# Performance work log

Measured on AMD Instinct MI355X. Metric: run time of the kernel, lower is better.

Reference implementation:

```python
import jax, jax.numpy as jnp
import numpy as np

N_HEAD = 9
HEAD_DIM = 64
KV_PER_HEAD = 21  # 189 // 9
ROPE_BASE = 10000.0


def _rotate_half(x):
    # matches torch: x1 = first half (floor), x2 = rest; cat(-x2, x1)
    h = x.shape[-1] // 2
    return jnp.concatenate([-x[..., h:], x[..., :h]], axis=-1)


def _rope_cos_sin(T, dtype):
    inv_freq = 1.0 / (ROPE_BASE ** (jnp.arange(0, KV_PER_HEAD, 2, dtype=jnp.float32) / KV_PER_HEAD))  # [11]
    t = jnp.arange(T, dtype=jnp.float32)
    freqs = jnp.einsum('i,j->ij', t, inv_freq)          # [T, 11]
    emb = jnp.concatenate([freqs, freqs], axis=-1)      # [T, 22]
    cos = jnp.cos(emb)[:, :KV_PER_HEAD].astype(dtype)   # [T, 21]
    sin = jnp.sin(emb)[:, :KV_PER_HEAD].astype(dtype)
    return cos, sin


def setup_inputs() -> dict:
    key = jax.random.key(0)
    ks = jax.random.split(key, 5)
    B, T, C = 4, 2048, 576
    kv_dim = 189
    s = 0.02
    return {
        'x': jax.random.normal(ks[0], (B, T, C), dtype=jnp.float32),
        'Wq': jax.random.normal(ks[1], (C, C), dtype=jnp.float32) * s,
        'Wk': jax.random.normal(ks[2], (C, kv_dim), dtype=jnp.float32) * s,
        'Wv': jax.random.normal(ks[3], (C, kv_dim), dtype=jnp.float32) * s,
        'Wo': jax.random.normal(ks[4], (C, C), dtype=jnp.float32) * s,
    }


def reference(x, Wq, Wk, Wv, Wo):
    B, T, C = x.shape
    q = (x @ Wq).reshape(B, T, N_HEAD, HEAD_DIM).transpose(0, 2, 1, 3)      # [B,H,T,64]
    k = (x @ Wk).reshape(B, T, N_HEAD, KV_PER_HEAD).transpose(0, 2, 1, 3)   # [B,H,T,21]
    v = (x @ Wv).reshape(B, T, N_HEAD, KV_PER_HEAD).transpose(0, 2, 1, 3)   # [B,H,T,21]

    cos, sin = _rope_cos_sin(T, x.dtype)  # [T,21] each, broadcasts over B,H
    k_rot = k * cos + _rotate_half(k) * sin
    q_part = q[..., :KV_PER_HEAD]
    q_rot_part = q_part * cos + _rotate_half(q_part) * sin
    # q dims >= KV_PER_HEAD never touch nonzero K, so only the first 21 dims matter
    scale = 1.0 / np.sqrt(HEAD_DIM)
    scores = jnp.einsum('bhqd,bhkd->bhqk', q_rot_part, k_rot) * scale       # [B,H,T,T]
    causal = jnp.tril(jnp.ones((T, T), dtype=bool))
    scores = jnp.where(causal, scores, -1e9)
    attn = jax.nn.softmax(scores, axis=-1)
    y_small = jnp.einsum('bhqk,bhkd->bhqd', attn, v)                        # [B,H,T,21]
    # zero-pad up to head_dim (matches k_pad/v_pad construction)
    y = jnp.pad(y_small, ((0, 0), (0, 0), (0, 0), (0, HEAD_DIM - KV_PER_HEAD)))
    y = y.transpose(0, 2, 1, 3).reshape(B, T, C)
    return y @ Wo
```

## Files before the change

### kernel.cpp

```cpp
#include <hip/hip_runtime.h>
#include <hip/hip_bf16.h>

typedef unsigned short u16;
typedef unsigned int u32;
typedef __attribute__((ext_vector_type(8))) short bf16x8;
typedef __attribute__((ext_vector_type(4))) float f32x4;
typedef __attribute__((ext_vector_type(4))) int i32x4;

#define N_HEADS 9
#define T_SEQ 2048
#define BATCH 4
#define CDIM 576
#define ROWS (BATCH * T_SEQ)
#define NBH (BATCH * N_HEADS)
#define PART_SLOT ((size_t)NBH * T_SEQ * 32)

__device__ __forceinline__ u16 f2bf(float f) {
    u32 u = __float_as_uint(f);
    u32 r = u + 0x7FFFu + ((u >> 16) & 1u);
    return (u16)(r >> 16);
}
__device__ __forceinline__ float bf2f(u16 u) { return __uint_as_float(((u32)u) << 16); }
__device__ __forceinline__ u32 cvt_pk_bf16(float lo, float hi) {
    u32 r;
    asm("v_cvt_pk_bf16_f32 %0, %1, %2" : "=v"(r) : "v"(lo), "v"(hi));
    return r;
}
__device__ __forceinline__ float exp2_raw(float x) {
    float r;
    asm("v_exp_f32 %0, %1" : "=v"(r) : "v"(x));
    return r;
}

__global__ __launch_bounds__(256) void prep_wt(const float* __restrict__ Wq, const float* __restrict__ Wk,
                                               const float* __restrict__ Wv, const float* __restrict__ Wo,
                                               u16* __restrict__ WcT, u16* __restrict__ WoSubT,
                                               float* __restrict__ cosT, float* __restrict__ sinT) {
    int idx = blockIdx.x * 256 + threadIdx.x;
    if (idx < 576 * 576) {
        int n = idx / 576, k = idx - n * 576;
        float v;
        if (n < 189)      v = Wq[(size_t)k * 576 + (n / 21) * 64 + (n % 21)];
        else if (n < 378) v = Wk[(size_t)k * 189 + (n - 189)];
        else if (n < 567) v = Wv[(size_t)k * 189 + (n - 378)];
        else              v = 0.f;
        WcT[(size_t)n * 576 + k] = f2bf(v);
    }
    if (idx < 576 * 192) {
        int n = idx / 192, k = idx - n * 192;
        float v = 0.f;
        if (k < 189) v = Wo[(size_t)((k / 21) * 64 + (k % 21)) * 576 + n];
        WoSubT[(size_t)n * 192 + k] = f2bf(v);
    }
    if (idx < T_SEQ * 21) {
        int t = idx / 21, d = idx - t * 21;
        int i = (d < 11) ? d : d - 11;
        float e = (2.0f * (float)i) / 21.0f;
        float invf = exp2f(-e * 13.287712379549449f);
        float ang = (float)t * invf;
        cosT[idx] = cosf(ang);
        sinT[idx] = sinf(ang);
    }
}


template <int AF32, int OUTF32>
__global__ __launch_bounds__(256) void gemm_mfma(const void* __restrict__ Av, const u16* __restrict__ BT,
                                                 void* __restrict__ Cout, int K, int lda, int ldbt, int ldc) {
    __shared__ u16 As[128][32];
    __shared__ u16 Bs[64][32];
    const int tid = threadIdx.x;
    const int lane = tid & 63, w = tid >> 6;
    const int m0 = blockIdx.x * 128, n0 = blockIdx.y * 64;
    const int k15 = lane & 15, g = lane >> 4;

    const int arow = tid >> 1;
    const int ac0 = (tid & 1) * 2;
    const int brow = tid >> 2, bc = tid & 3;

    f32x4 zero = {0.f, 0.f, 0.f, 0.f};
    f32x4 acc[2][4];
#pragma unroll
    for (int hf = 0; hf < 2; hf++)
#pragma unroll
        for (int n = 0; n < 4; n++) acc[hf][n] = zero;

    const float* Af = (const float*)Av;
    const u16*   Ab = (const u16*)Av;

    float4 af0, af1, af2, af3;
    i32x4 av0, av1;
    if (AF32) {
        const float* ap = &Af[(size_t)(m0 + arow) * lda + ac0 * 8];
        af0 = *(const float4*)&ap[0];
        af1 = *(const float4*)&ap[4];
        af2 = *(const float4*)&ap[8];
        af3 = *(const float4*)&ap[12];
    } else {
        av0 = *(const i32x4*)&Ab[(size_t)(m0 + arow) * lda + ac0 * 8];
        av1 = *(const i32x4*)&Ab[(size_t)(m0 + arow) * lda + (ac0 + 1) * 8];
    }
    i32x4 bv = *(const i32x4*)&BT[(size_t)(n0 + brow) * ldbt + bc * 8];

    for (int k0 = 0; k0 < K; k0 += 32) {
        __syncthreads();
        if (AF32) {
            i32x4 w0, w1;
            w0[0] = (int)cvt_pk_bf16(af0.x, af0.y); w0[1] = (int)cvt_pk_bf16(af0.z, af0.w);
            w0[2] = (int)cvt_pk_bf16(af1.x, af1.y); w0[3] = (int)cvt_pk_bf16(af1.z, af1.w);
            w1[0] = (int)cvt_pk_bf16(af2.x, af2.y); w1[1] = (int)cvt_pk_bf16(af2.z, af2.w);
            w1[2] = (int)cvt_pk_bf16(af3.x, af3.y); w1[3] = (int)cvt_pk_bf16(af3.z, af3.w);
            *(i32x4*)&As[arow][(ac0 ^ (arow & 3)) * 8] = w0;
            *(i32x4*)&As[arow][((ac0 + 1) ^ (arow & 3)) * 8] = w1;
        } else {
            *(i32x4*)&As[arow][(ac0 ^ (arow & 3)) * 8] = av0;
            *(i32x4*)&As[arow][((ac0 + 1) ^ (arow & 3)) * 8] = av1;
        }
        *(i32x4*)&Bs[brow][(bc ^ (brow & 3)) * 8] = bv;
        __syncthreads();
        int k1 = k0 + 32;
        if (k1 < K) {
            if (AF32) {
                const float* ap = &Af[(size_t)(m0 + arow) * lda + k1 + ac0 * 8];
                af0 = *(const float4*)&ap[0];
                af1 = *(const float4*)&ap[4];
                af2 = *(const float4*)&ap[8];
                af3 = *(const float4*)&ap[12];
            } else {
                av0 = *(const i32x4*)&Ab[(size_t)(m0 + arow) * lda + k1 + ac0 * 8];
                av1 = *(const i32x4*)&Ab[(size_t)(m0 + arow) * lda + k1 + (ac0 + 1) * 8];
            }
            bv = *(const i32x4*)&BT[(size_t)(n0 + brow) * ldbt + k1 + bc * 8];
        }
        const int ar0 = w * 32 + k15;
        bf16x8 a0 = *(const bf16x8*)&As[ar0][(g ^ (ar0 & 3)) * 8];
        bf16x8 a1 = *(const bf16x8*)&As[ar0 + 16][(g ^ (ar0 & 3)) * 8];
#pragma unroll
        for (int n = 0; n < 4; n++) {
            int br = n * 16 + k15;
            bf16x8 b = *(const bf16x8*)&Bs[br][(g ^ (br & 3)) * 8];
            acc[0][n] = __builtin_amdgcn_mfma_f32_16x16x32_bf16(a0, b, acc[0][n], 0, 0, 0);
            acc[1][n] = __builtin_amdgcn_mfma_f32_16x16x32_bf16(a1, b, acc[1][n], 0, 0, 0);
        }
    }
#pragma unroll
    for (int hf = 0; hf < 2; hf++)
#pragma unroll
        for (int n = 0; n < 4; n++)
#pragma unroll
            for (int i = 0; i < 4; i++) {
                int row = m0 + w * 32 + hf * 16 + g * 4 + i;
                int col = n0 + n * 16 + k15;
                float v = acc[hf][n][i];
                if (OUTF32) ((float*)Cout)[(size_t)row * ldc + col] = v;
                else        ((u16*)Cout)[(size_t)row * ldc + col] = f2bf(v);
            }
}


__global__ __launch_bounds__(256) void repack_qk(const u16* __restrict__ qkv,
                                                 const float* __restrict__ cosT,
                                                 const float* __restrict__ sinT,
                                                 u16* __restrict__ Qp, u16* __restrict__ Kp) {
    int gid = blockIdx.x * 256 + threadIdx.x;
    int c = gid & 3;
    int t = (gid >> 2) & 2047;
    int bh = gid >> 13;
    int b = bh / N_HEADS, h = bh - b * N_HEADS;
    const u16* qrow = qkv + (size_t)(b * T_SEQ + t) * CDIM + h * 21;
    const u16* krow = qrow + 189;
    const float* cr = cosT + t * 21;
    const float* sr = sinT + t * 21;
    u32 wq[4] = {0, 0, 0, 0}, wk[4] = {0, 0, 0, 0};
    const float sc = 0.18033688011112042f;
#pragma unroll
    for (int j = 0; j < 8; j++) {
        int d = c * 8 + j;
        float vq = 0.f, vk = 0.f;
        if (d < 21) {
            int pd = (d < 11) ? d + 10 : d - 11;
            float cc = cr[d], ss = sr[d];
            float qv = bf2f(qrow[d]), qp = bf2f(qrow[pd]);
            float kv = bf2f(krow[d]), kp = bf2f(krow[pd]);
            float rq = (d < 11) ? -qp : qp;
            float rk = (d < 11) ? -kp : kp;
            vq = (qv * cc + rq * ss) * sc;
            vk = kv * cc + rk * ss;
        }
        wq[j >> 1] |= (u32)f2bf(vq) << ((j & 1) * 16);
        wk[j >> 1] |= (u32)f2bf(vk) << ((j & 1) * 16);
    }
    size_t obase = ((size_t)bh * T_SEQ + t) * 32 + c * 8;
    i32x4 q4; q4[0] = (int)wq[0]; q4[1] = (int)wq[1]; q4[2] = (int)wq[2]; q4[3] = (int)wq[3];
    i32x4 k4; k4[0] = (int)wk[0]; k4[1] = (int)wk[1]; k4[2] = (int)wk[2]; k4[3] = (int)wk[3];
    *(i32x4*)&Qp[obase] = q4;
    *(i32x4*)&Kp[obase] = k4;
}

__global__ __launch_bounds__(256) void repack_v(const u16* __restrict__ qkv, u16* __restrict__ Vp) {
    __shared__ u16 Vs[256][26];
    const int tid = threadIdx.x;
    const int bh = blockIdx.y;
    const int b = bh / N_HEADS, h = bh - b * N_HEADS;
    const int t0 = blockIdx.x * 256;

    const u16* src = qkv + (size_t)(b * T_SEQ + t0 + tid) * CDIM + 378 + h * 21;
#pragma unroll
    for (int d = 0; d < 21; d++) Vs[tid][d] = src[d];
    __syncthreads();

    const int d = tid >> 3, tc = tid & 7;
    u32 wv[16];
#pragma unroll
    for (int j = 0; j < 32; j += 2) {
        u16 lo, hi;
        if (d < 21)      { lo = Vs[tc * 32 + j][d]; hi = Vs[tc * 32 + j + 1][d]; }
        else if (d == 31){ lo = 0x3F80; hi = 0x3F80; }
        else             { lo = 0; hi = 0; }
        wv[j >> 1] = (u32)lo | ((u32)hi << 16);
    }
    u16* dst = &Vp[((size_t)bh * 32 + d) * T_SEQ + t0 + tc * 32];
#pragma unroll
    for (int q = 0; q < 4; q++) {
        i32x4 v4; v4[0] = (int)wv[q*4]; v4[1] = (int)wv[q*4+1]; v4[2] = (int)wv[q*4+2]; v4[3] = (int)wv[q*4+3];
        *(i32x4*)&dst[q * 8] = v4;
    }
}


__global__ __launch_bounds__(256) void attn_mfma(const u16* __restrict__ Qp,
                                                 const u16* __restrict__ Kp,
                                                 const u16* __restrict__ Vp,
                                                 u16* __restrict__ Ybuf,
                                                 u16* __restrict__ Part) {
    __shared__ u16 Ks[128][40];
    __shared__ u16 Vt[32][136];
    __shared__ u16 Pt[4][16][72];
    const int tid = threadIdx.x;
    const int lane = tid & 63, w = tid >> 6;
    const int bh = blockIdx.y;
    const int b = bh / N_HEADS, h = bh - b * N_HEADS;
    const int k15 = lane & 15, g = lane >> 4;

    int bx = blockIdx.x, qt, ci;
    if (bx < 32) { qt = 31 - (bx >> 1); ci = bx & 1; }
    else         { qt = 47 - bx;        ci = 0;      }
    const int q0 = qt * 64;
    const int n64 = qt + 1;
    const int n128 = (n64 + 1) >> 1;
    int u_begin, u_end;
    if (qt < 16) { u_begin = 0; u_end = n128; }
    else { int c0 = (n128 + 1) >> 1; u_begin = ci ? c0 : 0; u_end = ci ? n128 : c0; }

    const u16* Kg = Kp + (((size_t)bh << 11) * 32) + (tid >> 1) * 32 + (tid & 1) * 16;
    const u16* Vg = Vp + (size_t)bh * 32 * T_SEQ + (size_t)(tid >> 3) * T_SEQ + (tid & 7) * 16;
    const int krow = tid >> 1, kcc = (tid & 1) * 16;
    const int vrow = tid >> 3, vcc = (tid & 7) * 16;

    bf16x8 qf = *(const bf16x8*)&Qp[(((size_t)bh << 11) + q0 + w * 16 + k15) * 32 + g * 8];

    f32x4 y0 = {0.f, 0.f, 0.f, 0.f}, y1 = {0.f, 0.f, 0.f, 0.f};
    const int qloc = w * 16 + k15;

    u32 ko = (u32)u_begin * 4096u;
    u32 vo = (u32)u_begin * 128u;
    i32x4 ka0 = *(const i32x4*)&Kg[ko];
    i32x4 ka1 = *(const i32x4*)&Kg[ko + 8];
    i32x4 va0 = *(const i32x4*)&Vg[vo];
    i32x4 va1 = *(const i32x4*)&Vg[vo + 8];

    for (int u = u_begin; u < u_end; ++u) {
        __syncthreads();
        *(i32x4*)&Ks[krow][kcc] = ka0;
        *(i32x4*)&Ks[krow][kcc + 8] = ka1;
        *(i32x4*)&Vt[vrow][vcc] = va0;
        *(i32x4*)&Vt[vrow][vcc + 8] = va1;
        if (u + 1 < u_end) {
            ko += 4096u; vo += 128u;
            ka0 = *(const i32x4*)&Kg[ko];
            ka1 = *(const i32x4*)&Kg[ko + 8];
            va0 = *(const i32x4*)&Vg[vo];
            va1 = *(const i32x4*)&Vg[vo + 8];
        }
        __syncthreads();

#pragma unroll
        for (int sub = 0; sub < 2; ++sub) {
            const int kt64 = u * 2 + sub;
            if (kt64 <= qt) {
                f32x4 s[4];
#pragma unroll
                for (int f = 0; f < 4; f++) {
                    bf16x8 kf = *(const bf16x8*)&Ks[sub * 64 + f * 16 + k15][g * 8];
                    f32x4 z = {0.f, 0.f, 0.f, 0.f};
                    s[f] = __builtin_amdgcn_mfma_f32_16x16x32_bf16(kf, qf, z, 0, 0, 0);
                }
                if (kt64 == qt) {
#pragma unroll
                    for (int f = 0; f < 4; f++)
#pragma unroll
                        for (int i = 0; i < 4; i++)
                            if (f * 16 + g * 4 + i > qloc) s[f][i] = -16384.f;
                }
#pragma unroll
                for (int f = 0; f < 4; f++) {
                    u32 lo = cvt_pk_bf16(exp2_raw(s[f][0]), exp2_raw(s[f][1]));
                    u32 hi = cvt_pk_bf16(exp2_raw(s[f][2]), exp2_raw(s[f][3]));
                    uint2 pk; pk.x = lo; pk.y = hi;
                    *(uint2*)&Pt[w][k15][f * 16 + g * 4] = pk;
                }
                asm volatile("" ::: "memory");
#pragma unroll
                for (int kh = 0; kh < 2; kh++) {
                    bf16x8 pa = *(const bf16x8*)&Pt[w][k15][kh * 32 + g * 8];
                    bf16x8 v0 = *(const bf16x8*)&Vt[k15][sub * 64 + kh * 32 + g * 8];
                    bf16x8 v1 = *(const bf16x8*)&Vt[16 + k15][sub * 64 + kh * 32 + g * 8];
                    y0 = __builtin_amdgcn_mfma_f32_16x16x32_bf16(pa, v0, y0, 0, 0, 0);
                    y1 = __builtin_amdgcn_mfma_f32_16x16x32_bf16(pa, v1, y1, 0, 0, 0);
                }
                asm volatile("" ::: "memory");
            }
        }
    }

    if (qt < 16) {
#pragma unroll
        for (int i = 0; i < 4; i++) {
            float li = __shfl(y1[i], (lane & 48) + 15);
            float inv = 1.0f / li;
            int rowY = b * T_SEQ + q0 + w * 16 + g * 4 + i;
            u16* yr = &Ybuf[(size_t)rowY * 192 + h * 21];
            yr[k15] = f2bf(y0[i] * inv);
            if (k15 < 5) yr[16 + k15] = f2bf(y1[i] * inv);
        }
    } else {
#pragma unroll
        for (int i = 0; i < 4; i++) {
            size_t pb = (size_t)ci * PART_SLOT +
                        (((size_t)bh << 11) + q0 + w * 16 + g * 4 + i) * 32;
            Part[pb + k15] = f2bf(y0[i]);
            Part[pb + 16 + k15] = f2bf(y1[i]);
        }
    }
}

__global__ __launch_bounds__(256) void attn_reduce(const u16* __restrict__ Part, u16* __restrict__ Ybuf) {
    int gid = blockIdx.x * 256 + threadIdx.x;
    int d = gid & 31;
    int t = 1024 + ((gid >> 5) & 1023);
    int bh = gid >> 15;
    int b = bh / N_HEADS, h = bh - b * N_HEADS;
    size_t base = (((size_t)bh << 11) + t) * 32;
    float l = bf2f(Part[base + 31]) + bf2f(Part[PART_SLOT + base + 31]);
    if (d < 21) {
        float v = bf2f(Part[base + d]) + bf2f(Part[PART_SLOT + base + d]);
        Ybuf[(size_t)(b * T_SEQ + t) * 192 + h * 21 + d] = f2bf(v / l);
    }
}


extern "C" void kernel_launch(void* const* d_in, const int* in_sizes, int n_in,
                              void* d_out, int out_size, void* d_ws, size_t ws_size,
                              hipStream_t stream) {
    const float* x  = (const float*)d_in[0];
    const float* Wq = (const float*)d_in[1];
    const float* Wk = (const float*)d_in[2];
    const float* Wv = (const float*)d_in[3];
    const float* Wo = (const float*)d_in[4];
    float* out = (float*)d_out;

    char* p = (char*)d_ws;
    auto alloc = [&](size_t bytes) { char* r = p; p += (bytes + 255) & ~(size_t)255; return r; };
    u16*   QpKp   = (u16*)alloc((size_t)ROWS * CDIM * 2);
    u16*   qkv    = (u16*)alloc((size_t)ROWS * CDIM * 2);
    u16*   WcT    = (u16*)alloc((size_t)576 * 576 * 2);
    u16*   WoSubT = (u16*)alloc((size_t)576 * 192 * 2);
    float* cosT   = (float*)alloc((size_t)T_SEQ * 21 * 4);
    float* sinT   = (float*)alloc((size_t)T_SEQ * 21 * 4);
    u16*   Vp     = (u16*)alloc((size_t)NBH * 32 * T_SEQ * 2);
    u16*   Ybuf   = (u16*)alloc((size_t)ROWS * 192 * 2);

    u16* Qp = QpKp;
    u16* Kp = QpKp + (size_t)NBH * T_SEQ * 32;
    u16* Part = qkv;

    prep_wt<<<dim3((576 * 576 + 255) / 256), dim3(256), 0, stream>>>(Wq, Wk, Wv, Wo, WcT, WoSubT, cosT, sinT);

    gemm_mfma<1, 0><<<dim3(ROWS / 128, 576 / 64), dim3(256), 0, stream>>>((const void*)x, WcT, (void*)qkv, 576, 576, 576, 576);

    repack_qk<<<dim3(NBH * T_SEQ * 4 / 256), dim3(256), 0, stream>>>(qkv, cosT, sinT, Qp, Kp);
    repack_v<<<dim3(T_SEQ / 256, NBH), dim3(256), 0, stream>>>(qkv, Vp);

    attn_mfma<<<dim3(48, NBH), dim3(256), 0, stream>>>(Qp, Kp, Vp, Ybuf, Part);
    attn_reduce<<<dim3(NBH * 1024 * 32 / 256), dim3(256), 0, stream>>>(Part, Ybuf);

    gemm_mfma<0, 1><<<dim3(ROWS / 128, 576 / 64), dim3(256), 0, stream>>>((const void*)Ybuf, WoSubT, (void*)out, 192, 192, 192, 576);
}
```

Baseline: 95.65 us.

## Stage K/V via async global_load_lds double buffering with swizzled layouts and finer split

The K and V repack kernels now write each 128-key unit as a contiguous, XOR-swizzled 8 KB tile. The attention kernel then loads these tiles straight into double-buffered LDS with global_load_lds, replacing register round-trips and two full barriers per iteration with a vmcnt-based prefetch. The work split goes from up to two chunks per query tile to up to four, chosen by tile index, so the grid grows from 48 to 80 blocks per head. A dedicated Part buffer and a variable-count reduce combine the chunks. The GEMM grid axes are also swapped to change block rasterization, and the extra split adds partial writes and reduce traffic.

Measured after the change: 110.2 us. +15.2%, slower.

```diff
diff --git a/kernel.cpp b/kernel.cpp
--- a/kernel.cpp
+++ b/kernel.cpp
@@ -30,6 +30,11 @@
     float r;
     asm("v_exp_f32 %0, %1" : "=v"(r) : "v"(x));
     return r;
+}
+__device__ __forceinline__ void gll16(const void* g, void* l) {
+    using GP = const __attribute__((address_space(1))) unsigned int*;
+    using LP = __attribute__((address_space(3))) unsigned int*;
+    __builtin_amdgcn_global_load_lds((GP)g, (LP)l, 16, 0, 0);
 }
 
 __global__ __launch_bounds__(256) void prep_wt(const float* __restrict__ Wq, const float* __restrict__ Wk,
@@ -71,7 +76,7 @@
     __shared__ u16 Bs[64][32];
     const int tid = threadIdx.x;
     const int lane = tid & 63, w = tid >> 6;
-    const int m0 = blockIdx.x * 128, n0 = blockIdx.y * 64;
+    const int m0 = blockIdx.y * 128, n0 = blockIdx.x * 64;
     const int k15 = lane & 15, g = lane >> 4;
 
     const int arow = tid >> 1;
@@ -190,11 +195,12 @@
         wq[j >> 1] |= (u32)f2bf(vq) << ((j & 1) * 16);
         wk[j >> 1] |= (u32)f2bf(vk) << ((j & 1) * 16);
     }
-    size_t obase = ((size_t)bh * T_SEQ + t) * 32 + c * 8;
     i32x4 q4; q4[0] = (int)wq[0]; q4[1] = (int)wq[1]; q4[2] = (int)wq[2]; q4[3] = (int)wq[3];
     i32x4 k4; k4[0] = (int)wk[0]; k4[1] = (int)wk[1]; k4[2] = (int)wk[2]; k4[3] = (int)wk[3];
-    *(i32x4*)&Qp[obase] = q4;
-    *(i32x4*)&Kp[obase] = k4;
+    *(i32x4*)&Qp[((size_t)bh * T_SEQ + t) * 32 + c * 8] = q4;
+    int k = t & 127, u = t >> 7;
+    int ql = k * 4 + (c ^ ((k >> 2) & 3));
+    *(i32x4*)&Kp[(size_t)bh * 65536 + (size_t)u * 4096 + ql * 8] = k4;
 }
 
 __global__ __launch_bounds__(256) void repack_v(const u16* __restrict__ qkv, u16* __restrict__ Vp) {
@@ -219,11 +225,14 @@
         else             { lo = 0; hi = 0; }
         wv[j >> 1] = (u32)lo | ((u32)hi << 16);
     }
-    u16* dst = &Vp[((size_t)bh * 32 + d) * T_SEQ + t0 + tc * 32];
-#pragma unroll
-    for (int q = 0; q < 4; q++) {
-        i32x4 v4; v4[0] = (int)wv[q*4]; v4[1] = (int)wv[q*4+1]; v4[2] = (int)wv[q*4+2]; v4[3] = (int)wv[q*4+3];
-        *(i32x4*)&dst[q * 8] = v4;
+    const int unit = blockIdx.x * 2 + (tc >> 2);
+    u16* dstU = Vp + (size_t)bh * 65536 + (size_t)unit * 4096;
+#pragma unroll
+    for (int m = 0; m < 4; m++) {
+        int c = (tc & 3) * 4 + m;
+        int ql = d * 16 + (c ^ (d & 7));
+        i32x4 v4; v4[0] = (int)wv[m * 4]; v4[1] = (int)wv[m * 4 + 1]; v4[2] = (int)wv[m * 4 + 2]; v4[3] = (int)wv[m * 4 + 3];
+        *(i32x4*)&dstU[ql * 8] = v4;
     }
 }
 
@@ -233,8 +242,8 @@
                                                  const u16* __restrict__ Vp,
                                                  u16* __restrict__ Ybuf,
                                                  u16* __restrict__ Part) {
-    __shared__ u16 Ks[128][40];
-    __shared__ u16 Vt[32][136];
+    __shared__ u16 KsB[2][4096];
+    __shared__ u16 VsB[2][4096];
     __shared__ u16 Pt[4][16][72];
     const int tid = threadIdx.x;
     const int lane = tid & 63, w = tid >> 6;
@@ -243,47 +252,55 @@
     const int k15 = lane & 15, g = lane >> 4;
 
     int bx = blockIdx.x, qt, ci;
-    if (bx < 32) { qt = 31 - (bx >> 1); ci = bx & 1; }
-    else         { qt = 47 - bx;        ci = 0;      }
+    if (bx < 32)      { qt = 31 - (bx >> 2); ci = bx & 3; }
+    else if (bx < 56) { int r = bx - 32; int q3 = r / 3; qt = 23 - q3; ci = r - q3 * 3; }
+    else if (bx < 72) { int r = bx - 56; qt = 15 - (r >> 1); ci = r & 1; }
+    else              { qt = 79 - bx; ci = 0; }
     const int q0 = qt * 64;
-    const int n64 = qt + 1;
-    const int n128 = (n64 + 1) >> 1;
-    int u_begin, u_end;
-    if (qt < 16) { u_begin = 0; u_end = n128; }
-    else { int c0 = (n128 + 1) >> 1; u_begin = ci ? c0 : 0; u_end = ci ? n128 : c0; }
-
-    const u16* Kg = Kp + (((size_t)bh << 11) * 32) + (tid >> 1) * 32 + (tid & 1) * 16;
-    const u16* Vg = Vp + (size_t)bh * 32 * T_SEQ + (size_t)(tid >> 3) * T_SEQ + (tid & 7) * 16;
-    const int krow = tid >> 1, kcc = (tid & 1) * 16;
-    const int vrow = tid >> 3, vcc = (tid & 7) * 16;
+    const int n128 = (qt + 2) >> 1;
+    const int nc = (qt >> 3) + 1;
+    const int u_begin = (ci * n128) / nc;
+    const int u_end = ((ci + 1) * n128) / nc;
+
+    const char* KgU = (const char*)Kp + (size_t)bh * 131072;
+    const char* VgU = (const char*)Vp + (size_t)bh * 131072;
+    char* Kl0 = (char*)&KsB[0][0];
+    char* Vl0 = (char*)&VsB[0][0];
 
     bf16x8 qf = *(const bf16x8*)&Qp[(((size_t)bh << 11) + q0 + w * 16 + k15) * 32 + g * 8];
+
+    auto stage = [&](int u, int buf) {
+        size_t go = (size_t)u * 8192 + (size_t)(w * 2048 + lane * 16);
+        char* kl = Kl0 + buf * 8192 + w * 2048;
+        char* vl = Vl0 + buf * 8192 + w * 2048;
+        gll16(KgU + go, kl);
+        gll16(KgU + go + 1024, kl + 1024);
+        gll16(VgU + go, vl);
+        gll16(VgU + go + 1024, vl + 1024);
+    };
 
     f32x4 y0 = {0.f, 0.f, 0.f, 0.f}, y1 = {0.f, 0.f, 0.f, 0.f};
     const int qloc = w * 16 + k15;
-
-    u32 ko = (u32)u_begin * 4096u;
-    u32 vo = (u32)u_begin * 128u;
-    i32x4 ka0 = *(const i32x4*)&Kg[ko];
-    i32x4 ka1 = *(const i32x4*)&Kg[ko + 8];
-    i32x4 va0 = *(const i32x4*)&Vg[vo];
-    i32x4 va1 = *(const i32x4*)&Vg[vo + 8];
-
+    const int kb  = k15 * 64 + ((g ^ ((k15 >> 2) & 3)) * 16);
+    const int vb0 = k15 * 256 + (((0 * 4 + g) ^ (k15 & 7)) * 16);
+    const int vb1 = k15 * 256 + (((1 * 4 + g) ^ (k15 & 7)) * 16);
+
+    stage(u_begin, 0);
+    int cur = 0;
     for (int u = u_begin; u < u_end; ++u) {
-        __syncthreads();
-        *(i32x4*)&Ks[krow][kcc] = ka0;
-        *(i32x4*)&Ks[krow][kcc + 8] = ka1;
-        *(i32x4*)&Vt[vrow][vcc] = va0;
-        *(i32x4*)&Vt[vrow][vcc + 8] = va1;
+        __builtin_amdgcn_s_barrier();
+        asm volatile("" ::: "memory");
         if (u + 1 < u_end) {
-            ko += 4096u; vo += 128u;
-            ka0 = *(const i32x4*)&Kg[ko];
-            ka1 = *(const i32x4*)&Kg[ko + 8];
-            va0 = *(const i32x4*)&Vg[vo];
-            va1 = *(const i32x4*)&Vg[vo + 8];
-        }
-        __syncthreads();
-
+            stage(u + 1, cur ^ 1);
+            asm volatile("s_waitcnt vmcnt(4)" ::: "memory");
+        } else {
+            asm volatile("s_waitcnt vmcnt(0)" ::: "memory");
+        }
+        __builtin_amdgcn_s_barrier();
+        asm volatile("" ::: "memory");
+
+        const char* Kb = Kl0 + cur * 8192;
+        const char* Vb = Vl0 + cur * 8192;
 #pragma unroll
         for (int sub = 0; sub < 2; ++sub) {
             const int kt64 = u * 2 + sub;
@@ -291,7 +308,7 @@
                 f32x4 s[4];
 #pragma unroll
                 for (int f = 0; f < 4; f++) {
-                    bf16x8 kf = *(const bf16x8*)&Ks[sub * 64 + f * 16 + k15][g * 8];
+                    bf16x8 kf = *(const bf16x8*)(Kb + sub * 4096 + f * 1024 + kb);
                     f32x4 z = {0.f, 0.f, 0.f, 0.f};
                     s[f] = __builtin_amdgcn_mfma_f32_16x16x32_bf16(kf, qf, z, 0, 0, 0);
                 }
@@ -312,18 +329,20 @@
                 asm volatile("" ::: "memory");
 #pragma unroll
                 for (int kh = 0; kh < 2; kh++) {
+                    const int vb = kh ? vb1 : vb0;
                     bf16x8 pa = *(const bf16x8*)&Pt[w][k15][kh * 32 + g * 8];
-                    bf16x8 v0 = *(const bf16x8*)&Vt[k15][sub * 64 + kh * 32 + g * 8];
-                    bf16x8 v1 = *(const bf16x8*)&Vt[16 + k15][sub * 64 + kh * 32 + g * 8];
+                    bf16x8 v0 = *(const bf16x8*)(Vb + sub * 128 + vb);
+                    bf16x8 v1 = *(const bf16x8*)(Vb + sub * 128 + vb + 4096);
                     y0 = __builtin_amdgcn_mfma_f32_16x16x32_bf16(pa, v0, y0, 0, 0, 0);
                     y1 = __builtin_amdgcn_mfma_f32_16x16x32_bf16(pa, v1, y1, 0, 0, 0);
                 }
                 asm volatile("" ::: "memory");
             }
         }
-    }
-
-    if (qt < 16) {
+        cur ^= 1;
+    }
+
+    if (nc == 1) {
 #pragma unroll
         for (int i = 0; i < 4; i++) {
             float li = __shfl(y1[i], (lane & 48) + 15);
@@ -347,15 +366,19 @@
 __global__ __launch_bounds__(256) void attn_reduce(const u16* __restrict__ Part, u16* __restrict__ Ybuf) {
     int gid = blockIdx.x * 256 + threadIdx.x;
     int d = gid & 31;
-    int t = 1024 + ((gid >> 5) & 1023);
-    int bh = gid >> 15;
+    int rest = gid >> 5;
+    int t = 512 + (rest % 1536);
+    int bh = rest / 1536;
     int b = bh / N_HEADS, h = bh - b * N_HEADS;
+    int qt = t >> 6;
+    int nc = (qt >> 3) + 1;
     size_t base = (((size_t)bh << 11) + t) * 32;
-    float l = bf2f(Part[base + 31]) + bf2f(Part[PART_SLOT + base + 31]);
-    if (d < 21) {
-        float v = bf2f(Part[base + d]) + bf2f(Part[PART_SLOT + base + d]);
-        Ybuf[(size_t)(b * T_SEQ + t) * 192 + h * 21 + d] = f2bf(v / l);
-    }
+    float l = 0.f, v = 0.f;
+    for (int ci = 0; ci < nc; ci++) {
+        l += bf2f(Part[(size_t)ci * PART_SLOT + base + 31]);
+        if (d < 21) v += bf2f(Part[(size_t)ci * PART_SLOT + base + d]);
+    }
+    if (d < 21) Ybuf[(size_t)(b * T_SEQ + t) * 192 + h * 21 + d] = f2bf(v / l);
 }
 
 
@@ -377,22 +400,22 @@
     u16*   WoSubT = (u16*)alloc((size_t)576 * 192 * 2);
     float* cosT   = (float*)alloc((size_t)T_SEQ * 21 * 4);
     float* sinT   = (float*)alloc((size_t)T_SEQ * 21 * 4);
-    u16*   Vp     = (u16*)alloc((size_t)NBH * 32 * T_SEQ * 2);
+    u16*   Vp     = (u16*)alloc((size_t)NBH * 16 * 4096 * 2);
     u16*   Ybuf   = (u16*)alloc((size_t)ROWS * 192 * 2);
+    u16*   Part   = (u16*)alloc((size_t)4 * PART_SLOT * 2);
 
     u16* Qp = QpKp;
     u16* Kp = QpKp + (size_t)NBH * T_SEQ * 32;
-    u16* Part = qkv;
 
     prep_wt<<<dim3((576 * 576 + 255) / 256), dim3(256), 0, stream>>>(Wq, Wk, Wv, Wo, WcT, WoSubT, cosT, sinT);
 
-    gemm_mfma<1, 0><<<dim3(ROWS / 128, 576 / 64), dim3(256), 0, stream>>>((const void*)x, WcT, (void*)qkv, 576, 576, 576, 576);
+    gemm_mfma<1, 0><<<dim3(576 / 64, ROWS / 128), dim3(256), 0, stream>>>((const void*)x, WcT, (void*)qkv, 576, 576, 576, 576);
 
     repack_qk<<<dim3(NBH * T_SEQ * 4 / 256), dim3(256), 0, stream>>>(qkv, cosT, sinT, Qp, Kp);
     repack_v<<<dim3(T_SEQ / 256, NBH), dim3(256), 0, stream>>>(qkv, Vp);
 
-    attn_mfma<<<dim3(48, NBH), dim3(256), 0, stream>>>(Qp, Kp, Vp, Ybuf, Part);
-    attn_reduce<<<dim3(NBH * 1024 * 32 / 256), dim3(256), 0, stream>>>(Part, Ybuf);
-
-    gemm_mfma<0, 1><<<dim3(ROWS / 128, 576 / 64), dim3(256), 0, stream>>>((const void*)Ybuf, WoSubT, (void*)out, 192, 192, 192, 576);
-}
+    attn_mfma<<<dim3(80, NBH), dim3(256), 0, stream>>>(Qp, Kp, Vp, Ybuf, Part);
+    attn_reduce<<<dim3(NBH * 1536 * 32 / 256), dim3(256), 0, stream>>>(Part, Ybuf);
+
+    gemm_mfma<0, 1><<<dim3(576 / 64, ROWS / 128), dim3(256), 0, stream>>>((const void*)Ybuf, WoSubT, (void*)out, 192, 192, 192, 576);
+}
```

## Split long causal query tiles into up to four KV chunks and fuse QKV repack

Applied to the files above, without the earlier changes.

The attention launch now splits each query tile's KV range into up to four chunks, with the chunk count growing with tile index, so the grid grows from 48 to 80 blocks per batch-head and work per block is more even. The reduce kernel sums a variable number of partials, written to a dedicated Part buffer instead of aliasing qkv. The Q/K rope repack and the V transpose are merged into one kernel, and the GEMM grid is flattened to 1D so consecutive blocks walk along M. This trades more partial-sum traffic and workspace for better load balance and one fewer launch.

New measurement: 92.40 us. -3.4%, faster.

```diff
diff --git a/kernel.cpp b/kernel.cpp
--- a/kernel.cpp
+++ b/kernel.cpp
@@ -71,7 +71,7 @@
     __shared__ u16 Bs[64][32];
     const int tid = threadIdx.x;
     const int lane = tid & 63, w = tid >> 6;
-    const int m0 = blockIdx.x * 128, n0 = blockIdx.y * 64;
+    const int m0 = (blockIdx.x & 63) * 128, n0 = (blockIdx.x >> 6) * 64;
     const int k15 = lane & 15, g = lane >> 4;
 
     const int arow = tid >> 1;
@@ -158,17 +158,25 @@
 }
 
 
-__global__ __launch_bounds__(256) void repack_qk(const u16* __restrict__ qkv,
-                                                 const float* __restrict__ cosT,
-                                                 const float* __restrict__ sinT,
-                                                 u16* __restrict__ Qp, u16* __restrict__ Kp) {
-    int gid = blockIdx.x * 256 + threadIdx.x;
-    int c = gid & 3;
-    int t = (gid >> 2) & 2047;
-    int bh = gid >> 13;
-    int b = bh / N_HEADS, h = bh - b * N_HEADS;
+__global__ __launch_bounds__(256) void repack_qkv(const u16* __restrict__ qkv,
+                                                  const float* __restrict__ cosT,
+                                                  const float* __restrict__ sinT,
+                                                  u16* __restrict__ Qp, u16* __restrict__ Kp,
+                                                  u16* __restrict__ Vp) {
+    __shared__ u16 Vs[64][26];
+    const int tid = threadIdx.x;
+    const int bh = blockIdx.y;
+    const int b = bh / N_HEADS, h = bh - b * N_HEADS;
+    const int t0 = blockIdx.x * 64;
+    const int r = tid >> 2, c = tid & 3;
+    const int t = t0 + r;
+
     const u16* qrow = qkv + (size_t)(b * T_SEQ + t) * CDIM + h * 21;
     const u16* krow = qrow + 189;
+    const u16* vrow = krow + 189;
+
+    for (int d = c * 6; d < c * 6 + 6 && d < 21; ++d) Vs[r][d] = vrow[d];
+
     const float* cr = cosT + t * 21;
     const float* sr = sinT + t * 21;
     u32 wq[4] = {0, 0, 0, 0}, wk[4] = {0, 0, 0, 0};
@@ -195,36 +203,21 @@
     i32x4 k4; k4[0] = (int)wk[0]; k4[1] = (int)wk[1]; k4[2] = (int)wk[2]; k4[3] = (int)wk[3];
     *(i32x4*)&Qp[obase] = q4;
     *(i32x4*)&Kp[obase] = k4;
-}
-
-__global__ __launch_bounds__(256) void repack_v(const u16* __restrict__ qkv, u16* __restrict__ Vp) {
-    __shared__ u16 Vs[256][26];
-    const int tid = threadIdx.x;
-    const int bh = blockIdx.y;
-    const int b = bh / N_HEADS, h = bh - b * N_HEADS;
-    const int t0 = blockIdx.x * 256;
-
-    const u16* src = qkv + (size_t)(b * T_SEQ + t0 + tid) * CDIM + 378 + h * 21;
-#pragma unroll
-    for (int d = 0; d < 21; d++) Vs[tid][d] = src[d];
+
     __syncthreads();
 
     const int d = tid >> 3, tc = tid & 7;
-    u32 wv[16];
-#pragma unroll
-    for (int j = 0; j < 32; j += 2) {
+    u32 wv[4];
+#pragma unroll
+    for (int j = 0; j < 4; j++) {
         u16 lo, hi;
-        if (d < 21)      { lo = Vs[tc * 32 + j][d]; hi = Vs[tc * 32 + j + 1][d]; }
+        if (d < 21)      { lo = Vs[tc * 8 + j * 2][d]; hi = Vs[tc * 8 + j * 2 + 1][d]; }
         else if (d == 31){ lo = 0x3F80; hi = 0x3F80; }
         else             { lo = 0; hi = 0; }
-        wv[j >> 1] = (u32)lo | ((u32)hi << 16);
-    }
-    u16* dst = &Vp[((size_t)bh * 32 + d) * T_SEQ + t0 + tc * 32];
-#pragma unroll
-    for (int q = 0; q < 4; q++) {
-        i32x4 v4; v4[0] = (int)wv[q*4]; v4[1] = (int)wv[q*4+1]; v4[2] = (int)wv[q*4+2]; v4[3] = (int)wv[q*4+3];
-        *(i32x4*)&dst[q * 8] = v4;
-    }
+        wv[j] = (u32)lo | ((u32)hi << 16);
+    }
+    i32x4 v4; v4[0] = (int)wv[0]; v4[1] = (int)wv[1]; v4[2] = (int)wv[2]; v4[3] = (int)wv[3];
+    *(i32x4*)&Vp[((size_t)bh * 32 + d) * T_SEQ + t0 + tc * 8] = v4;
 }
 
 
@@ -243,14 +236,15 @@
     const int k15 = lane & 15, g = lane >> 4;
 
     int bx = blockIdx.x, qt, ci;
-    if (bx < 32) { qt = 31 - (bx >> 1); ci = bx & 1; }
-    else         { qt = 47 - bx;        ci = 0;      }
+    if (bx < 32)      { qt = 31 - (bx >> 2); ci = bx & 3; }
+    else if (bx < 56) { int r = bx - 32; int q3 = r / 3; qt = 23 - q3; ci = r - q3 * 3; }
+    else if (bx < 72) { int r = bx - 56; qt = 15 - (r >> 1); ci = r & 1; }
+    else              { qt = 79 - bx; ci = 0; }
     const int q0 = qt * 64;
-    const int n64 = qt + 1;
-    const int n128 = (n64 + 1) >> 1;
-    int u_begin, u_end;
-    if (qt < 16) { u_begin = 0; u_end = n128; }
-    else { int c0 = (n128 + 1) >> 1; u_begin = ci ? c0 : 0; u_end = ci ? n128 : c0; }
+    const int n128 = (qt + 2) >> 1;
+    const int nc = (qt >> 3) + 1;
+    const int u_begin = (ci * n128) / nc;
+    const int u_end = ((ci + 1) * n128) / nc;
 
     const u16* Kg = Kp + (((size_t)bh << 11) * 32) + (tid >> 1) * 32 + (tid & 1) * 16;
     const u16* Vg = Vp + (size_t)bh * 32 * T_SEQ + (size_t)(tid >> 3) * T_SEQ + (tid & 7) * 16;
@@ -323,7 +317,7 @@
         }
     }
 
-    if (qt < 16) {
+    if (nc == 1) {
 #pragma unroll
         for (int i = 0; i < 4; i++) {
             float li = __shfl(y1[i], (lane & 48) + 15);
@@ -347,15 +341,19 @@
 __global__ __launch_bounds__(256) void attn_reduce(const u16* __restrict__ Part, u16* __restrict__ Ybuf) {
     int gid = blockIdx.x * 256 + threadIdx.x;
     int d = gid & 31;
-    int t = 1024 + ((gid >> 5) & 1023);
-    int bh = gid >> 15;
+    int rest = gid >> 5;
+    int t = 512 + (rest % 1536);
+    int bh = rest / 1536;
     int b = bh / N_HEADS, h = bh - b * N_HEADS;
+    int qt = t >> 6;
+    int nc = (qt >> 3) + 1;
     size_t base = (((size_t)bh << 11) + t) * 32;
-    float l = bf2f(Part[base + 31]) + bf2f(Part[PART_SLOT + base + 31]);
-    if (d < 21) {
-        float v = bf2f(Part[base + d]) + bf2f(Part[PART_SLOT + base + d]);
-        Ybuf[(size_t)(b * T_SEQ + t) * 192 + h * 21 + d] = f2bf(v / l);
-    }
+    float l = 0.f, v = 0.f;
+    for (int ci = 0; ci < nc; ci++) {
+        l += bf2f(Part[(size_t)ci * PART_SLOT + base + 31]);
+        if (d < 21) v += bf2f(Part[(size_t)ci * PART_SLOT + base + d]);
+    }
+    if (d < 21) Ybuf[(size_t)(b * T_SEQ + t) * 192 + h * 21 + d] = f2bf(v / l);
 }
 
 
@@ -379,20 +377,19 @@
     float* sinT   = (float*)alloc((size_t)T_SEQ * 21 * 4);
     u16*   Vp     = (u16*)alloc((size_t)NBH * 32 * T_SEQ * 2);
     u16*   Ybuf   = (u16*)alloc((size_t)ROWS * 192 * 2);
+    u16*   Part   = (u16*)alloc((size_t)4 * PART_SLOT * 2);
 
     u16* Qp = QpKp;
     u16* Kp = QpKp + (size_t)NBH * T_SEQ * 32;
-    u16* Part = qkv;
 
     prep_wt<<<dim3((576 * 576 + 255) / 256), dim3(256), 0, stream>>>(Wq, Wk, Wv, Wo, WcT, WoSubT, cosT, sinT);
 
-    gemm_mfma<1, 0><<<dim3(ROWS / 128, 576 / 64), dim3(256), 0, stream>>>((const void*)x, WcT, (void*)qkv, 576, 576, 576, 576);
-
-    repack_qk<<<dim3(NBH * T_SEQ * 4 / 256), dim3(256), 0, stream>>>(qkv, cosT, sinT, Qp, Kp);
-    repack_v<<<dim3(T_SEQ / 256, NBH), dim3(256), 0, stream>>>(qkv, Vp);
-
-    attn_mfma<<<dim3(48, NBH), dim3(256), 0, stream>>>(Qp, Kp, Vp, Ybuf, Part);
-    attn_reduce<<<dim3(NBH * 1024 * 32 / 256), dim3(256), 0, stream>>>(Part, Ybuf);
-
-    gemm_mfma<0, 1><<<dim3(ROWS / 128, 576 / 64), dim3(256), 0, stream>>>((const void*)Ybuf, WoSubT, (void*)out, 192, 192, 192, 576);
-}
+    gemm_mfma<1, 0><<<dim3(64 * 9), dim3(256), 0, stream>>>((const void*)x, WcT, (void*)qkv, 576, 576, 576, 576);
+
+    repack_qkv<<<dim3(T_SEQ / 64, NBH), dim3(256), 0, stream>>>(qkv, cosT, sinT, Qp, Kp, Vp);
+
+    attn_mfma<<<dim3(80, NBH), dim3(256), 0, stream>>>(Qp, Kp, Vp, Ybuf, Part);
+    attn_reduce<<<dim3(NBH * 1536 * 32 / 256), dim3(256), 0, stream>>>(Part, Ybuf);
+
+    gemm_mfma<0, 1><<<dim3(64 * 9), dim3(256), 0, stream>>>((const void*)Ybuf, WoSubT, (void*)out, 192, 192, 192, 576);
+}
```
